# Optimization experiments

Hardware: AMD Instinct MI355X
Metric: run time of the kernel (lower is better)

Reference implementation:

```python
import jax, jax.numpy as jnp
import numpy as np

TIME_STEPS = 100
SPIKE_THRESHOLD = 0.5
INPUT_DIM = 8192


def setup_inputs() -> dict:
    key = jax.random.key(0)
    k_x, k_w = jax.random.split(key)
    x = jax.random.uniform(k_x, (INPUT_DIM,), dtype=jnp.float32)
    # matches nn.Parameter(torch.rand(D, D) * 0.01)
    synaptic_weights = jax.random.uniform(k_w, (INPUT_DIM, INPUT_DIM), dtype=jnp.float32) * 0.01
    # matches nn.Parameter(torch.zeros(D))
    membrane_potential = jnp.zeros((INPUT_DIM,), dtype=jnp.float32)
    return {"x": x, "synaptic_weights": synaptic_weights, "membrane_potential": membrane_potential}


def reference(x, synaptic_weights, membrane_potential):
    # Drive is identical every timestep (x and W are loop-invariant), so compute once.
    drive = x @ synaptic_weights  # [D]

    def step(pot, _):
        pot = pot + drive
        spike = (pot >= SPIKE_THRESHOLD).astype(pot.dtype)  # spike_mask.float()
        pot = pot * (1.0 - spike)  # membrane_potential[spike_mask] = 0
        return pot, (spike, pot)

    _, (spikes, potentials) = jax.lax.scan(step, membrane_potential, None, length=TIME_STEPS)
    synaptic_activity = jnp.abs(synaptic_weights).mean()
    # spikes: [T, D], potentials: [T, D], synaptic_activity: scalar
    return spikes, potentials, synaptic_activity
```

## Files before the change

### kernel.cpp

```cpp
#include <hip/hip_runtime.h>

#define D 8192
#define T_STEPS 100
#define SPIKE_THR 0.5f
#define BLOCK 256
#define WAVES (BLOCK / 64)
#define COLS_PER_THREAD 4
#define NCHUNK 256
#define ROWS_PER_CHUNK (D / NCHUNK)
#define COLBLOCKS (D / (BLOCK * COLS_PER_THREAD))
#define NABS (NCHUNK * COLBLOCKS * WAVES)

#define RED_COLS 64
#define RED_SEGS (BLOCK / RED_COLS)
#define RED_BLOCKS (D / RED_COLS)
#define CHUNKS_PER_SEG (NCHUNK / RED_SEGS)
#define STEPS_PER_SEG (T_STEPS / RED_SEGS)

__global__ void __launch_bounds__(BLOCK)
k_partial(const float* __restrict__ x, const float* __restrict__ W,
          float* __restrict__ ws_drive, float* __restrict__ ws_abs) {
    const int chunk = blockIdx.y;
    const int row0  = chunk * ROWS_PER_CHUNK;
    const int j0 = (blockIdx.x * BLOCK + threadIdx.x) * COLS_PER_THREAD;

    float ax = 0.f, ay = 0.f, az = 0.f, aw = 0.f;
    float asum = 0.f;
    #pragma unroll 8
    for (int i = 0; i < ROWS_PER_CHUNK; ++i) {
        const float xv = x[row0 + i];
        const float4 w = *reinterpret_cast<const float4*>(
            &W[(size_t)(row0 + i) * D + j0]);
        ax = fmaf(xv, w.x, ax);
        ay = fmaf(xv, w.y, ay);
        az = fmaf(xv, w.z, az);
        aw = fmaf(xv, w.w, aw);
        asum += fabsf(w.x) + fabsf(w.y) + fabsf(w.z) + fabsf(w.w);
    }

    float4 acc; acc.x = ax; acc.y = ay; acc.z = az; acc.w = aw;
    *reinterpret_cast<float4*>(&ws_drive[(size_t)chunk * D + j0]) = acc;

    #pragma unroll
    for (int off = 32; off > 0; off >>= 1)
        asum += __shfl_down(asum, off, 64);
    if ((threadIdx.x & 63) == 0)
        ws_abs[(chunk * COLBLOCKS + blockIdx.x) * WAVES + (threadIdx.x >> 6)] = asum;
}

__global__ void __launch_bounds__(BLOCK)
k_fused(const float* __restrict__ ws_drive, const float* __restrict__ ws_abs,
        const float* __restrict__ pot0, float* __restrict__ out) {
    if (blockIdx.x == RED_BLOCKS) {
        __shared__ float red[BLOCK];
        float s = 0.f;
        for (int i = threadIdx.x; i < NABS; i += BLOCK) s += ws_abs[i];
        red[threadIdx.x] = s;
        __syncthreads();
        for (int st = BLOCK / 2; st > 0; st >>= 1) {
            if (threadIdx.x < st) red[threadIdx.x] += red[threadIdx.x + st];
            __syncthreads();
        }
        if (threadIdx.x == 0)
            out[(size_t)2 * T_STEPS * D] = red[0] / ((float)D * (float)D);
        return;
    }

    __shared__ float part[RED_SEGS][RED_COLS];
    const int col = threadIdx.x & (RED_COLS - 1);
    const int seg = threadIdx.x >> 6;
    const int j   = blockIdx.x * RED_COLS + col;

    float s = 0.f;
    const int c0 = seg * CHUNKS_PER_SEG;
    #pragma unroll 8
    for (int cc = 0; cc < CHUNKS_PER_SEG; ++cc)
        s += ws_drive[(size_t)(c0 + cc) * D + j];
    part[seg][col] = s;
    __syncthreads();

    const float d = part[0][col] + part[1][col] + part[2][col] + part[3][col];
    float p = pot0[j];

    const int t0 = seg * STEPS_PER_SEG;
    for (int t = 0; t < t0; ++t) {
        p += d;
        p = (p >= SPIKE_THR) ? 0.f : p;
    }

    float* __restrict__ spikes = out;
    float* __restrict__ pots   = out + (size_t)T_STEPS * D;

    #pragma unroll
    for (int s2 = 0; s2 < STEPS_PER_SEG; ++s2) {
        const int t = t0 + s2;
        p += d;
        const float sp = (p >= SPIKE_THR) ? 1.f : 0.f;
        p *= (1.f - sp);
        spikes[(size_t)t * D + j] = sp;
        pots[(size_t)t * D + j]   = p;
    }
}

extern "C" void kernel_launch(void* const* d_in, const int* in_sizes, int n_in,
                              void* d_out, int out_size, void* d_ws, size_t ws_size,
                              hipStream_t stream) {
    const float* x   = (const float*)d_in[0];
    const float* W   = (const float*)d_in[1];
    const float* mp0 = (const float*)d_in[2];
    float* out = (float*)d_out;

    float* ws_drive = (float*)d_ws;
    float* ws_abs   = ws_drive + (size_t)NCHUNK * D;

    dim3 g1(COLBLOCKS, NCHUNK);
    k_partial<<<g1, BLOCK, 0, stream>>>(x, W, ws_drive, ws_abs);
    k_fused<<<RED_BLOCKS + 1, BLOCK, 0, stream>>>(ws_drive, ws_abs, mp0, out);
}
```

Baseline: 55.62 us.

## Restructure partial GEMV so each block covers full rows with 16 columns per thread

The partial-drive kernel now assigns each 512-thread block a 16-row chunk spanning all 8192 columns, with each thread loading four float4s per row at stride 2048. This replaces the 2D grid of 256-column-chunk blocks and doubles NCHUNK to 512. The aim is more independent loads in flight per thread and fewer, larger blocks that each read contiguous full rows. The cost is a twice-as-large ws_drive workspace that the reduction kernel must read, and fewer rows per chunk to amortize per-block overhead.

```diff
diff --git a/kernel.cpp b/kernel.cpp
--- a/kernel.cpp
+++ b/kernel.cpp
@@ -3,49 +3,65 @@
 #define D 8192
 #define T_STEPS 100
 #define SPIKE_THR 0.5f
+
+#define BLOCK1 512
+#define WAVES1 (BLOCK1 / 64)
+#define NCHUNK 512
+#define ROWS_PER_CHUNK (D / NCHUNK)
+#define SEGS 4
+#define NABS (NCHUNK * WAVES1)
+
 #define BLOCK 256
-#define WAVES (BLOCK / 64)
-#define COLS_PER_THREAD 4
-#define NCHUNK 256
-#define ROWS_PER_CHUNK (D / NCHUNK)
-#define COLBLOCKS (D / (BLOCK * COLS_PER_THREAD))
-#define NABS (NCHUNK * COLBLOCKS * WAVES)
-
 #define RED_COLS 64
 #define RED_SEGS (BLOCK / RED_COLS)
 #define RED_BLOCKS (D / RED_COLS)
 #define CHUNKS_PER_SEG (NCHUNK / RED_SEGS)
 #define STEPS_PER_SEG (T_STEPS / RED_SEGS)
 
-__global__ void __launch_bounds__(BLOCK)
+__global__ void __launch_bounds__(BLOCK1)
 k_partial(const float* __restrict__ x, const float* __restrict__ W,
           float* __restrict__ ws_drive, float* __restrict__ ws_abs) {
-    const int chunk = blockIdx.y;
+    const int chunk = blockIdx.x;
     const int row0  = chunk * ROWS_PER_CHUNK;
-    const int j0 = (blockIdx.x * BLOCK + threadIdx.x) * COLS_PER_THREAD;
+    const int t4    = threadIdx.x * 4;
 
-    float ax = 0.f, ay = 0.f, az = 0.f, aw = 0.f;
+    float4 a0 = {0.f,0.f,0.f,0.f}, a1 = {0.f,0.f,0.f,0.f};
+    float4 a2 = {0.f,0.f,0.f,0.f}, a3 = {0.f,0.f,0.f,0.f};
     float asum = 0.f;
-    #pragma unroll 8
-    for (int i = 0; i < ROWS_PER_CHUNK; ++i) {
-        const float xv = x[row0 + i];
-        const float4 w = *reinterpret_cast<const float4*>(
-            &W[(size_t)(row0 + i) * D + j0]);
-        ax = fmaf(xv, w.x, ax);
-        ay = fmaf(xv, w.y, ay);
-        az = fmaf(xv, w.z, az);
-        aw = fmaf(xv, w.w, aw);
-        asum += fabsf(w.x) + fabsf(w.y) + fabsf(w.z) + fabsf(w.w);
+
+    #pragma unroll 2
+    for (int r = 0; r < ROWS_PER_CHUNK; ++r) {
+        const float xv = x[row0 + r];
+        const float* Wr = &W[(size_t)(row0 + r) * D + t4];
+        const float4 w0 = *reinterpret_cast<const float4*>(Wr);
+        const float4 w1 = *reinterpret_cast<const float4*>(Wr + 2048);
+        const float4 w2 = *reinterpret_cast<const float4*>(Wr + 4096);
+        const float4 w3 = *reinterpret_cast<const float4*>(Wr + 6144);
+        a0.x = fmaf(xv, w0.x, a0.x); a0.y = fmaf(xv, w0.y, a0.y);
+        a0.z = fmaf(xv, w0.z, a0.z); a0.w = fmaf(xv, w0.w, a0.w);
+        a1.x = fmaf(xv, w1.x, a1.x); a1.y = fmaf(xv, w1.y, a1.y);
+        a1.z = fmaf(xv, w1.z, a1.z); a1.w = fmaf(xv, w1.w, a1.w);
+        a2.x = fmaf(xv, w2.x, a2.x); a2.y = fmaf(xv, w2.y, a2.y);
+        a2.z = fmaf(xv, w2.z, a2.z); a2.w = fmaf(xv, w2.w, a2.w);
+        a3.x = fmaf(xv, w3.x, a3.x); a3.y = fmaf(xv, w3.y, a3.y);
+        a3.z = fmaf(xv, w3.z, a3.z); a3.w = fmaf(xv, w3.w, a3.w);
+        asum += fabsf(w0.x) + fabsf(w0.y) + fabsf(w0.z) + fabsf(w0.w)
+              + fabsf(w1.x) + fabsf(w1.y) + fabsf(w1.z) + fabsf(w1.w)
+              + fabsf(w2.x) + fabsf(w2.y) + fabsf(w2.z) + fabsf(w2.w)
+              + fabsf(w3.x) + fabsf(w3.y) + fabsf(w3.z) + fabsf(w3.w);
     }
 
-    float4 acc; acc.x = ax; acc.y = ay; acc.z = az; acc.w = aw;
-    *reinterpret_cast<float4*>(&ws_drive[(size_t)chunk * D + j0]) = acc;
+    float* wd = &ws_drive[(size_t)chunk * D + t4];
+    *reinterpret_cast<float4*>(wd)        = a0;
+    *reinterpret_cast<float4*>(wd + 2048) = a1;
+    *reinterpret_cast<float4*>(wd + 4096) = a2;
+    *reinterpret_cast<float4*>(wd + 6144) = a3;
 
     #pragma unroll
     for (int off = 32; off > 0; off >>= 1)
         asum += __shfl_down(asum, off, 64);
     if ((threadIdx.x & 63) == 0)
-        ws_abs[(chunk * COLBLOCKS + blockIdx.x) * WAVES + (threadIdx.x >> 6)] = asum;
+        ws_abs[chunk * WAVES1 + (threadIdx.x >> 6)] = asum;
 }
 
 __global__ void __launch_bounds__(BLOCK)
@@ -113,7 +129,6 @@
     float* ws_drive = (float*)d_ws;
     float* ws_abs   = ws_drive + (size_t)NCHUNK * D;
 
-    dim3 g1(COLBLOCKS, NCHUNK);
-    k_partial<<<g1, BLOCK, 0, stream>>>(x, W, ws_drive, ws_abs);
+    k_partial<<<NCHUNK, BLOCK1, 0, stream>>>(x, W, ws_drive, ws_abs);
     k_fused<<<RED_BLOCKS + 1, BLOCK, 0, stream>>>(ws_drive, ws_abs, mp0, out);
 }
```

New measurement: 59.22 us. 6.5% more time.
